# Kernel tuning notes

Measured on AMD Instinct MI355X. Metric: run time of the kernel, lower is better.

Reference implementation:

```python
import jax, jax.numpy as jnp
import numpy as np

B, M, FIN, K, FOUT, NNZ = 8, 40000, 64, 6, 64, 320000

def setup_inputs() -> dict:
    key = jax.random.key(0)
    k1, k2, k3, k4, k5 = jax.random.split(key, 5)
    x = jax.random.normal(k1, (B, M, FIN), dtype=jnp.float32)
    edge_rows = jax.random.randint(k2, (NNZ,), 0, M)
    edge_cols = jax.random.randint(k3, (NNZ,), 0, M)
    edge_vals = jax.random.normal(k4, (NNZ,), dtype=jnp.float32) * 0.1
    W = jax.random.normal(k5, (FIN * K, FOUT), dtype=jnp.float32) * 0.05
    return {"x": x, "edge_vals": edge_vals, "W": W,
            "edge_rows": edge_rows, "edge_cols": edge_cols}

def reference(x, edge_vals, W, edge_rows, edge_cols):
    Bd, Md, Fin = x.shape
    nK = W.shape[0] // Fin
    Fout = W.shape[1]
    # x0: [M, Fin*B] as in tf.transpose([1,2,0]) + reshape
    x0 = jnp.transpose(x, (1, 2, 0)).reshape(Md, Fin * Bd)

    def spmm_rescaled(v):
        # rescale_L(L, lmax=2) = L - I, so (L - I) @ v = L@v - v
        Lv = jax.ops.segment_sum(edge_vals[:, None] * v[edge_cols],
                                 edge_rows, num_segments=Md)
        return Lv - v

    xs = [x0]
    if nK > 1:
        x1 = spmm_rescaled(x0)
        xs.append(x1)
        xp, xc = x0, x1
        for _ in range(2, nK):
            xn = 2.0 * spmm_rescaled(xc) - xp  # Chebyshev recurrence
            xs.append(xn)
            xp, xc = xc, xn
    X = jnp.stack(xs, axis=0)                     # [K, M, Fin*B]
    X = X.reshape(nK, Md, Fin, Bd)                # split Fin*B -> (Fin, B)
    X = jnp.transpose(X, (3, 1, 2, 0))            # [B, M, Fin, K]
    X = X.reshape(Bd * Md, Fin * nK)
    out = (X @ W).reshape(Bd, Md, Fout)           # dense projection
    return out
```

## Files before the change

### kernel.cpp

```cpp
#include <hip/hip_runtime.h>

#define Mn    40000
#define Bn    8
#define FINn  64
#define Kn    6
#define FOUTn 64
#define NNZn  320000
#define Cn    512
#define NB    ((Mn + 255) / 256)


typedef _Float16 half8 __attribute__((ext_vector_type(8)));
typedef __attribute__((ext_vector_type(4))) float floatx4;

__device__ __forceinline__ ushort f2h(float f) {
    _Float16 h = (_Float16)f;
    return *(ushort*)&h;
}


__global__ __launch_bounds__(256) void k_hist(const int* __restrict__ rows,
                                              int* __restrict__ cnt) {
    int e = blockIdx.x * 256 + threadIdx.x;
    if (e < NNZn) atomicAdd(&cnt[rows[e]], 1);
}

__global__ __launch_bounds__(256) void k_scan_part(const int* __restrict__ cnt,
                                                   int* __restrict__ rowptr,
                                                   int* __restrict__ bsum) {
    __shared__ int part[256];
    int tid = threadIdx.x;
    int r = blockIdx.x * 256 + tid;
    int v = (r < Mn) ? cnt[r] : 0;
    part[tid] = v;
    __syncthreads();
    for (int off = 1; off < 256; off <<= 1) {
        int t = (tid >= off) ? part[tid - off] : 0;
        __syncthreads();
        part[tid] += t;
        __syncthreads();
    }
    if (r < Mn) rowptr[r] = part[tid] - v;
    if (tid == 255) bsum[blockIdx.x] = part[255];
}

__global__ __launch_bounds__(256) void k_scan_bsums(const int* __restrict__ bsum,
                                                    int* __restrict__ boff,
                                                    int* __restrict__ rowptr) {
    __shared__ int part[256];
    int tid = threadIdx.x;
    int v = (tid < NB) ? bsum[tid] : 0;
    part[tid] = v;
    __syncthreads();
    for (int off = 1; off < 256; off <<= 1) {
        int t = (tid >= off) ? part[tid - off] : 0;
        __syncthreads();
        part[tid] += t;
        __syncthreads();
    }
    if (tid < NB) boff[tid] = part[tid] - v;
    if (tid == 255) rowptr[Mn] = part[255];
}

__global__ __launch_bounds__(256) void k_scan_add(int* __restrict__ rowptr,
                                                  const int* __restrict__ boff) {
    int r = blockIdx.x * 256 + threadIdx.x;
    if (r < Mn) rowptr[r] += boff[blockIdx.x];
}

__global__ __launch_bounds__(256) void k_scatter(const int* __restrict__ rows,
                                                 const int* __restrict__ cols,
                                                 const float* __restrict__ vals,
                                                 const int* __restrict__ rowptr,
                                                 int* __restrict__ fill,
                                                 int2* __restrict__ csr) {
    int e = blockIdx.x * 256 + threadIdx.x;
    if (e < NNZn) {
        int r = rows[e];
        int p = rowptr[r] + atomicAdd(&fill[r], 1);
        int2 cv; cv.x = cols[e]; cv.y = __float_as_int(vals[e]);
        csr[p] = cv;
    }
}


__global__ __launch_bounds__(256) void k_transpose_h(const float* __restrict__ x,
                                                     ushort* __restrict__ x0h) {
    size_t i = ((size_t)blockIdx.x * 256 + threadIdx.x) * 8;
    float4 a = *(const float4*)(x + i);
    float4 b = *(const float4*)(x + i + 4);
    union { uint4 u; ushort h[8]; } s;
    s.h[0] = f2h(a.x); s.h[1] = f2h(a.y); s.h[2] = f2h(a.z); s.h[3] = f2h(a.w);
    s.h[4] = f2h(b.x); s.h[5] = f2h(b.y); s.h[6] = f2h(b.z); s.h[7] = f2h(b.w);
    *(uint4*)(x0h + i) = s.u;
}


__device__ __forceinline__ void fmah8(float* a, uint4 g, float w) {
    union { uint4 u; _Float16 h[8]; } c; c.u = g;
#pragma unroll
    for (int i = 0; i < 8; ++i) a[i] += w * (float)c.h[i];
}

__global__ __launch_bounds__(256) void k_spmm_h(const ushort* __restrict__ xc,
                                                const ushort* __restrict__ xp,
                                                ushort* __restrict__ xn,
                                                const int* __restrict__ rowptr,
                                                const int2* __restrict__ csr,
                                                int first) {
    int t = threadIdx.x;
    int lane = t & 63;
    int m = blockIdx.x * 4 + (t >> 6);
    const uint4* xc4 = (const uint4*)xc;
    size_t loff = (size_t)(lane >> 3) * ((size_t)Mn * 8) + (lane & 7);
    uint4 v = xc4[loff + (size_t)m * 8];
    float a[8];
    { union { uint4 u; _Float16 h[8]; } c; c.u = v;
#pragma unroll
      for (int i = 0; i < 8; ++i) a[i] = -(float)c.h[i]; }

    int e = rowptr[m], end = rowptr[m + 1];
    for (; e + 8 <= end; e += 8) {
        int2 cv[8];
#pragma unroll
        for (int i = 0; i < 8; ++i) cv[i] = csr[e + i];
        uint4 g[8];
#pragma unroll
        for (int i = 0; i < 8; ++i) g[i] = xc4[loff + (size_t)cv[i].x * 8];
#pragma unroll
        for (int i = 0; i < 8; ++i) fmah8(a, g[i], __int_as_float(cv[i].y));
    }
    for (; e + 4 <= end; e += 4) {
        int2 cv0 = csr[e],     cv1 = csr[e + 1];
        int2 cv2 = csr[e + 2], cv3 = csr[e + 3];
        uint4 g0 = xc4[loff + (size_t)cv0.x * 8];
        uint4 g1 = xc4[loff + (size_t)cv1.x * 8];
        uint4 g2 = xc4[loff + (size_t)cv2.x * 8];
        uint4 g3 = xc4[loff + (size_t)cv3.x * 8];
        fmah8(a, g0, __int_as_float(cv0.y));
        fmah8(a, g1, __int_as_float(cv1.y));
        fmah8(a, g2, __int_as_float(cv2.y));
        fmah8(a, g3, __int_as_float(cv3.y));
    }
    for (; e < end; ++e) {
        int2 cv = csr[e];
        uint4 g = xc4[loff + (size_t)cv.x * 8];
        fmah8(a, g, __int_as_float(cv.y));
    }

    if (!first) {
        uint4 p = ((const uint4*)xp)[loff + (size_t)m * 8];
        union { uint4 u; _Float16 h[8]; } c; c.u = p;
#pragma unroll
        for (int i = 0; i < 8; ++i) a[i] = 2.f * a[i] - (float)c.h[i];
    }
    union { uint4 u; _Float16 h[8]; } s;
#pragma unroll
    for (int i = 0; i < 8; ++i) s.h[i] = (_Float16)a[i];
    ((uint4*)xn)[loff + (size_t)m * 8] = s.u;
}


__global__ __launch_bounds__(256) void k_wfrag(const float* __restrict__ W,
                                               ushort* __restrict__ wfrag) {
    int idx = blockIdx.x * 256 + threadIdx.x;
    if (idx >= 12 * 4 * 64 * 8) return;
    int j    = idx & 7;
    int lane = (idx >> 3) & 63;
    int n    = (idx >> 9) & 3;
    int kk   = idx >> 11;
    int k    = (lane >> 4) * 8 + j;
    int lev  = kk >> 1;
    int f    = (kk & 1) * 32 + k;
    int fo   = n * 16 + (lane & 15);
    wfrag[idx] = f2h(W[(f * Kn + lev) * FOUTn + fo]);
}


__global__ __launch_bounds__(256) void k_gemm_mfma(const ushort* __restrict__ xh,
                                                   const ushort* __restrict__ wfrag,
                                                   float* __restrict__ out) {
    __shared__ __align__(16) ushort As[64 * 64];
    int t    = threadIdx.x;
    int wv   = t >> 6;
    int lane = t & 63;
    int q    = lane >> 4, r = lane & 15;
    int b    = blockIdx.x & 7;
    int m0   = (blockIdx.x >> 3) * 64;

    int srow0 = t >> 3, spart = t & 7;
    int srow1 = srow0 + 32;
    const size_t lstride4 = (size_t)Bn * Mn * 8;
    size_t gbase4 = (((size_t)b * Mn + m0) * 64) / 8;
    const uint4* xh4 = (const uint4*)xh;
    const uint4* src0 = xh4 + gbase4 + (size_t)srow0 * 8 + spart;
    const uint4* src1 = xh4 + gbase4 + (size_t)srow1 * 8 + spart;
    int d0 = srow0 * 128 + ((spart * 16) ^ ((srow0 & 7) << 4));
    int d1 = srow1 * 128 + ((spart * 16) ^ ((srow1 & 7) << 4));

    int row  = wv * 16 + r;
    int asw  = row & 7;
    int abase = row * 64;

    floatx4 acc[4];
    acc[0] = (floatx4)0.f; acc[1] = (floatx4)0.f;
    acc[2] = (floatx4)0.f; acc[3] = (floatx4)0.f;

    uint4 v0 = src0[0];
    uint4 v1 = src1[0];
#pragma unroll
    for (int lev = 0; lev < 6; ++lev) {
        __syncthreads();
        *(uint4*)((char*)As + d0) = v0;
        *(uint4*)((char*)As + d1) = v1;
        if (lev < 5) {
            v0 = src0[(lev + 1) * lstride4];
            v1 = src1[(lev + 1) * lstride4];
        }
        __syncthreads();
#pragma unroll
        for (int half = 0; half < 2; ++half) {
            half8 af = *(const half8*)&As[abase + ((((half * 4) + q) ^ asw) << 3)];
            int kkg = lev * 2 + half;
            const ushort* wf = wfrag + ((size_t)(kkg * 4) * 64 + lane) * 8;
            acc[0] = __builtin_amdgcn_mfma_f32_16x16x32_f16(af, *(const half8*)(wf),        acc[0], 0, 0, 0);
            acc[1] = __builtin_amdgcn_mfma_f32_16x16x32_f16(af, *(const half8*)(wf + 512),  acc[1], 0, 0, 0);
            acc[2] = __builtin_amdgcn_mfma_f32_16x16x32_f16(af, *(const half8*)(wf + 1024), acc[2], 0, 0, 0);
            acc[3] = __builtin_amdgcn_mfma_f32_16x16x32_f16(af, *(const half8*)(wf + 1536), acc[3], 0, 0, 0);
        }
    }

    size_t obase = ((size_t)b * Mn + m0 + wv * 16) * FOUTn;
#pragma unroll
    for (int n = 0; n < 4; ++n) {
#pragma unroll
        for (int reg = 0; reg < 4; ++reg) {
            int orow = q * 4 + reg;
            out[obase + (size_t)orow * FOUTn + n * 16 + r] = acc[n][reg];
        }
    }
}


__global__ __launch_bounds__(512) void k_transpose_f(const float* __restrict__ x,
                                                     float* __restrict__ x0) {
    int m = blockIdx.x, t = threadIdx.x;
    int b = t >> 6, f = t & 63;
    x0[(size_t)m * Cn + t] = x[((size_t)b * Mn + m) * 64 + f];
}

__global__ __launch_bounds__(256) void k_spmm_f32(const float4* __restrict__ xc,
                                                  const float4* __restrict__ xp,
                                                  float4* __restrict__ xn,
                                                  const int* __restrict__ rowptr,
                                                  const int2* __restrict__ csr,
                                                  int first) {
    int t = threadIdx.x;
    int lane = t & 63;
    int m = blockIdx.x * 4 + (t >> 6);
    size_t rb = (size_t)m * 128;
    float4 v0 = xc[rb + lane];
    float4 v1 = xc[rb + 64 + lane];
    float4 a0 = make_float4(-v0.x, -v0.y, -v0.z, -v0.w);
    float4 a1 = make_float4(-v1.x, -v1.y, -v1.z, -v1.w);
    int e = rowptr[m], end = rowptr[m + 1];
    for (; e < end; ++e) {
        int2 cv = csr[e];
        float w = __int_as_float(cv.y);
        const float4* r = xc + (size_t)cv.x * 128;
        float4 g0 = r[lane], g1 = r[64 + lane];
        a0.x += w * g0.x; a0.y += w * g0.y; a0.z += w * g0.z; a0.w += w * g0.w;
        a1.x += w * g1.x; a1.y += w * g1.y; a1.z += w * g1.z; a1.w += w * g1.w;
    }
    if (!first) {
        float4 p0 = xp[rb + lane];
        float4 p1 = xp[rb + 64 + lane];
        a0.x = 2.f * a0.x - p0.x; a0.y = 2.f * a0.y - p0.y;
        a0.z = 2.f * a0.z - p0.z; a0.w = 2.f * a0.w - p0.w;
        a1.x = 2.f * a1.x - p1.x; a1.y = 2.f * a1.y - p1.y;
        a1.z = 2.f * a1.z - p1.z; a1.w = 2.f * a1.w - p1.w;
    }
    xn[rb + lane] = a0;
    xn[rb + 64 + lane] = a1;
}

__global__ __launch_bounds__(256) void k_gemm2(const float* __restrict__ xa,
                                               const float* __restrict__ xb,
                                               const float* __restrict__ W,
                                               float* __restrict__ out,
                                               int ka, int kb, int accum) {
    __shared__ __align__(16) float Wa[64 * 64];
    __shared__ __align__(16) float Wb[64 * 64];
    __shared__ __align__(16) float xsa[4 * Cn];
    __shared__ __align__(16) float xsb[4 * Cn];
    int t = threadIdx.x;
    size_t m0 = (size_t)blockIdx.x * 4;
    for (int i = t; i < 4096; i += 256) {
        int f = i >> 6, fo = i & 63;
        Wa[i] = W[(f * Kn + ka) * FOUTn + fo];
        Wb[i] = W[(f * Kn + kb) * FOUTn + fo];
    }
    for (int i = t; i < 4 * Cn; i += 256) {
        xsa[i] = xa[m0 * Cn + i];
        xsb[i] = xb[m0 * Cn + i];
    }
    __syncthreads();
    int fo  = (t & 15) * 4;
    int idx = t >> 4;
    int m   = idx & 3;
    int bq  = idx >> 2;
    float4 acc0 = make_float4(0.f, 0.f, 0.f, 0.f);
    float4 acc1 = make_float4(0.f, 0.f, 0.f, 0.f);
    for (int f = 0; f < 64; ++f) {
        float4 wa = *(const float4*)&Wa[f * 64 + fo];
        float a0 = xsa[m * Cn + bq * 64 + f];
        float a1 = xsa[m * Cn + (bq + 4) * 64 + f];
        acc0.x += a0 * wa.x; acc0.y += a0 * wa.y; acc0.z += a0 * wa.z; acc0.w += a0 * wa.w;
        acc1.x += a1 * wa.x; acc1.y += a1 * wa.y; acc1.z += a1 * wa.z; acc1.w += a1 * wa.w;
        float4 wb = *(const float4*)&Wb[f * 64 + fo];
        float b0 = xsb[m * Cn + bq * 64 + f];
        float b1 = xsb[m * Cn + (bq + 4) * 64 + f];
        acc0.x += b0 * wb.x; acc0.y += b0 * wb.y; acc0.z += b0 * wb.z; acc0.w += b0 * wb.w;
        acc1.x += b1 * wb.x; acc1.y += b1 * wb.y; acc1.z += b1 * wb.z; acc1.w += b1 * wb.w;
    }
    size_t o0 = (((size_t)bq * Mn) + (m0 + m)) * FOUTn + fo;
    size_t o1 = (((size_t)(bq + 4) * Mn) + (m0 + m)) * FOUTn + fo;
    float4* out4_0 = (float4*)&out[o0];
    float4* out4_1 = (float4*)&out[o1];
    if (accum) {
        float4 c0 = *out4_0, c1 = *out4_1;
        acc0.x += c0.x; acc0.y += c0.y; acc0.z += c0.z; acc0.w += c0.w;
        acc1.x += c1.x; acc1.y += c1.y; acc1.z += c1.z; acc1.w += c1.w;
    }
    *out4_0 = acc0;
    *out4_1 = acc1;
}


extern "C" void kernel_launch(void* const* d_in, const int* in_sizes, int n_in,
                              void* d_out, int out_size, void* d_ws, size_t ws_size,
                              hipStream_t stream) {
    const float* x         = (const float*)d_in[0];
    const float* edge_vals = (const float*)d_in[1];
    const float* W         = (const float*)d_in[2];
    const int*   edge_rows = (const int*)d_in[3];
    const int*   edge_cols = (const int*)d_in[4];
    float* out = (float*)d_out;

    char* ws = (char*)d_ws;
    const size_t bufB = (size_t)Mn * Cn * sizeof(float);
    const size_t bufH = (size_t)Mn * Cn * sizeof(ushort);
    const size_t wfB  = 12 * 4 * 64 * 8 * sizeof(ushort);
    const size_t csrB = (size_t)(Mn + 4 + Mn) * 4 + (size_t)NNZn * 8;

    const int spmm_grid = Mn / 4;
    const int gemm_grid = (Mn / 64) * 8;

    if (ws_size >= 6 * bufH + wfB + csrB) {
        ushort* xh  = (ushort*)ws;
        ushort* wfr = (ushort*)(ws + 6 * bufH);
        int*    rowptr = (int*)(ws + 6 * bufH + wfB);
        int*    fill   = rowptr + (Mn + 4);
        int2*   csr    = (int2*)(fill + Mn);
        int*    bsum   = (int*)csr;
        int*    boff   = bsum + 256;
        ushort* slot[6];
        for (int l = 0; l < 6; ++l) slot[l] = xh + (size_t)l * Mn * Cn;

        hipMemsetAsync(fill, 0, Mn * sizeof(int), stream);
        k_hist<<<(NNZn + 255) / 256, 256, 0, stream>>>(edge_rows, fill);
        k_scan_part<<<NB, 256, 0, stream>>>(fill, rowptr, bsum);
        k_scan_bsums<<<1, 256, 0, stream>>>(bsum, boff, rowptr);
        k_scan_add<<<NB, 256, 0, stream>>>(rowptr, boff);
        hipMemsetAsync(fill, 0, Mn * sizeof(int), stream);
        k_scatter<<<(NNZn + 255) / 256, 256, 0, stream>>>(edge_rows, edge_cols,
                                                          edge_vals, rowptr, fill, csr);
        k_wfrag<<<96, 256, 0, stream>>>(W, wfr);

        k_transpose_h<<<(Bn * Mn * FINn) / (256 * 8), 256, 0, stream>>>(x, slot[0]);
        k_spmm_h<<<spmm_grid, 256, 0, stream>>>(slot[0], slot[0], slot[1],
                                                rowptr, csr, 1);
        k_spmm_h<<<spmm_grid, 256, 0, stream>>>(slot[1], slot[0], slot[2],
                                                rowptr, csr, 0);
        k_spmm_h<<<spmm_grid, 256, 0, stream>>>(slot[2], slot[1], slot[3],
                                                rowptr, csr, 0);
        k_spmm_h<<<spmm_grid, 256, 0, stream>>>(slot[3], slot[2], slot[4],
                                                rowptr, csr, 0);
        k_spmm_h<<<spmm_grid, 256, 0, stream>>>(slot[4], slot[3], slot[5],
                                                rowptr, csr, 0);
        k_gemm_mfma<<<gemm_grid, 256, 0, stream>>>(xh, wfr, out);
    } else {
        float* buf0 = (float*)(ws);
        float* buf1 = (float*)(ws + bufB);
        float* buf2 = (float*)(ws + 2 * bufB);
        int*   rowptr = (int*)(ws + 3 * bufB);
        int*   fill   = rowptr + (Mn + 4);
        int2*  csr    = (int2*)(fill + Mn);
        int*   bsum   = (int*)csr;
        int*   boff   = bsum + 256;
        hipMemsetAsync(fill, 0, Mn * sizeof(int), stream);
        k_hist<<<(NNZn + 255) / 256, 256, 0, stream>>>(edge_rows, fill);
        k_scan_part<<<NB, 256, 0, stream>>>(fill, rowptr, bsum);
        k_scan_bsums<<<1, 256, 0, stream>>>(bsum, boff, rowptr);
        k_scan_add<<<NB, 256, 0, stream>>>(rowptr, boff);
        hipMemsetAsync(fill, 0, Mn * sizeof(int), stream);
        k_scatter<<<(NNZn + 255) / 256, 256, 0, stream>>>(edge_rows, edge_cols,
                                                          edge_vals, rowptr, fill, csr);
        k_transpose_f<<<Mn, 512, 0, stream>>>(x, buf0);
        k_spmm_f32<<<spmm_grid, 256, 0, stream>>>((const float4*)buf0, (const float4*)buf0,
                                                  (float4*)buf1, rowptr, csr, 1);
        k_gemm2<<<Mn / 4, 256, 0, stream>>>(buf0, buf1, W, out, 0, 1, 0);
        k_spmm_f32<<<spmm_grid, 256, 0, stream>>>((const float4*)buf1, (const float4*)buf0,
                                                  (float4*)buf2, rowptr, csr, 0);
        k_spmm_f32<<<spmm_grid, 256, 0, stream>>>((const float4*)buf2, (const float4*)buf1,
                                                  (float4*)buf0, rowptr, csr, 0);
        k_gemm2<<<Mn / 4, 256, 0, stream>>>(buf2, buf0, W, out, 2, 3, 1);
        k_spmm_f32<<<spmm_grid, 256, 0, stream>>>((const float4*)buf0, (const float4*)buf2,
                                                  (float4*)buf1, rowptr, csr, 0);
        k_spmm_f32<<<spmm_grid, 256, 0, stream>>>((const float4*)buf1, (const float4*)buf0,
                                                  (float4*)buf2, rowptr, csr, 0);
        k_gemm2<<<Mn / 4, 256, 0, stream>>>(buf1, buf2, W, out, 4, 5, 1);
    }
}
```

Baseline: 552.0 us.

## Fold scatter cursor init into scan, hoist loads in SpMM and GEMM

The scan-add kernel now also writes each row's start offset into a cursor array, so the scatter needs one atomic per edge and no second memset. The SpMM kernel issues the previous-level load at kernel start so it overlaps the gather loop. The GEMM kernel prefetches all six Chebyshev-level tiles into registers up front instead of double-buffering one level at a time. This adds register pressure that may lower occupancy.

```diff
diff --git a/kernel.cpp b/kernel.cpp
--- a/kernel.cpp
+++ b/kernel.cpp
@@ -63,21 +63,24 @@
 }
 
 __global__ __launch_bounds__(256) void k_scan_add(int* __restrict__ rowptr,
-                                                  const int* __restrict__ boff) {
+                                                  const int* __restrict__ boff,
+                                                  int* __restrict__ wcur) {
     int r = blockIdx.x * 256 + threadIdx.x;
-    if (r < Mn) rowptr[r] += boff[blockIdx.x];
+    if (r < Mn) {
+        int v = rowptr[r] + boff[blockIdx.x];
+        rowptr[r] = v;
+        wcur[r] = v;
+    }
 }
 
 __global__ __launch_bounds__(256) void k_scatter(const int* __restrict__ rows,
                                                  const int* __restrict__ cols,
                                                  const float* __restrict__ vals,
-                                                 const int* __restrict__ rowptr,
-                                                 int* __restrict__ fill,
+                                                 int* __restrict__ wcur,
                                                  int2* __restrict__ csr) {
     int e = blockIdx.x * 256 + threadIdx.x;
     if (e < NNZn) {
-        int r = rows[e];
-        int p = rowptr[r] + atomicAdd(&fill[r], 1);
+        int p = atomicAdd(&wcur[rows[e]], 1);
         int2 cv; cv.x = cols[e]; cv.y = __float_as_int(vals[e]);
         csr[p] = cv;
     }
@@ -114,6 +117,8 @@
     const uint4* xc4 = (const uint4*)xc;
     size_t loff = (size_t)(lane >> 3) * ((size_t)Mn * 8) + (lane & 7);
     uint4 v = xc4[loff + (size_t)m * 8];
+    uint4 p;
+    if (!first) p = ((const uint4*)xp)[loff + (size_t)m * 8];
     float a[8];
     { union { uint4 u; _Float16 h[8]; } c; c.u = v;
 #pragma unroll
@@ -149,7 +154,6 @@
     }
 
     if (!first) {
-        uint4 p = ((const uint4*)xp)[loff + (size_t)m * 8];
         union { uint4 u; _Float16 h[8]; } c; c.u = p;
 #pragma unroll
         for (int i = 0; i < 8; ++i) a[i] = 2.f * a[i] - (float)c.h[i];
@@ -206,17 +210,18 @@
     acc[0] = (floatx4)0.f; acc[1] = (floatx4)0.f;
     acc[2] = (floatx4)0.f; acc[3] = (floatx4)0.f;
 
-    uint4 v0 = src0[0];
-    uint4 v1 = src1[0];
+    uint4 va[6], vb[6];
 #pragma unroll
     for (int lev = 0; lev < 6; ++lev) {
-        __syncthreads();
-        *(uint4*)((char*)As + d0) = v0;
-        *(uint4*)((char*)As + d1) = v1;
-        if (lev < 5) {
-            v0 = src0[(lev + 1) * lstride4];
-            v1 = src1[(lev + 1) * lstride4];
-        }
+        va[lev] = src0[(size_t)lev * lstride4];
+        vb[lev] = src1[(size_t)lev * lstride4];
+    }
+
+#pragma unroll
+    for (int lev = 0; lev < 6; ++lev) {
+        __syncthreads();
+        *(uint4*)((char*)As + d0) = va[lev];
+        *(uint4*)((char*)As + d1) = vb[lev];
         __syncthreads();
 #pragma unroll
         for (int half = 0; half < 2; ++half) {
@@ -371,10 +376,9 @@
         k_hist<<<(NNZn + 255) / 256, 256, 0, stream>>>(edge_rows, fill);
         k_scan_part<<<NB, 256, 0, stream>>>(fill, rowptr, bsum);
         k_scan_bsums<<<1, 256, 0, stream>>>(bsum, boff, rowptr);
-        k_scan_add<<<NB, 256, 0, stream>>>(rowptr, boff);
-        hipMemsetAsync(fill, 0, Mn * sizeof(int), stream);
+        k_scan_add<<<NB, 256, 0, stream>>>(rowptr, boff, fill);
         k_scatter<<<(NNZn + 255) / 256, 256, 0, stream>>>(edge_rows, edge_cols,
-                                                          edge_vals, rowptr, fill, csr);
+                                                          edge_vals, fill, csr);
         k_wfrag<<<96, 256, 0, stream>>>(W, wfr);
 
         k_transpose_h<<<(Bn * Mn * FINn) / (256 * 8), 256, 0, stream>>>(x, slot[0]);
@@ -402,10 +406,9 @@
         k_hist<<<(NNZn + 255) / 256, 256, 0, stream>>>(edge_rows, fill);
         k_scan_part<<<NB, 256, 0, stream>>>(fill, rowptr, bsum);
         k_scan_bsums<<<1, 256, 0, stream>>>(bsum, boff, rowptr);
-        k_scan_add<<<NB, 256, 0, stream>>>(rowptr, boff);
-        hipMemsetAsync(fill, 0, Mn * sizeof(int), stream);
+        k_scan_add<<<NB, 256, 0, stream>>>(rowptr, boff, fill);
         k_scatter<<<(NNZn + 255) / 256, 256, 0, stream>>>(edge_rows, edge_cols,
-                                                          edge_vals, rowptr, fill, csr);
+                                                          edge_vals, fill, csr);
         k_transpose_f<<<Mn, 512, 0, stream>>>(x, buf0);
         k_spmm_f32<<<spmm_grid, 256, 0, stream>>>((const float4*)buf0, (const float4*)buf0,
                                                   (float4*)buf1, rowptr, csr, 1);
```

After: 635.1 us. 15.0% more time.
